# Performance work log

Measured on AMD Instinct MI355X. Metric: run time of the kernel, lower is better.

The kernel has to match this reference:

```python
import jax, jax.numpy as jnp
import numpy as np

B, S, E = 2, 2048, 2048
NQ, NKV, HD = 16, 4, 128
WINDOW = 512
ROPE_BASE = 10000.0


def _rope(x):
    # x: [B, H, S, HD], interleaved even/odd rotation
    half = HD // 2
    freqs = 1.0 / (ROPE_BASE ** (2.0 * jnp.arange(half, dtype=jnp.float32) / HD))
    pos = jnp.arange(x.shape[2], dtype=jnp.float32)
    ang = pos[:, None] * freqs[None, :]            # [S, HD/2]
    cos = jnp.cos(ang)[None, None].astype(x.dtype)  # [1,1,S,HD/2]
    sin = jnp.sin(ang)[None, None].astype(x.dtype)
    xe = x[..., 0::2]
    xo = x[..., 1::2]
    re = xe * cos - xo * sin
    ro = xe * sin + xo * cos
    return jnp.stack([re, ro], axis=-1).reshape(x.shape)


def setup_inputs() -> dict:
    key = jax.random.key(0)
    ks = jax.random.split(key, 9)
    s_in = 1.0 / np.sqrt(E)
    s_out = 1.0 / np.sqrt(NQ * HD)
    return {
        "x": jax.random.normal(ks[0], (B, S, E), jnp.float32),
        "Wq": jax.random.normal(ks[1], (E, NQ * HD), jnp.float32) * s_in,
        "bq": jax.random.normal(ks[2], (NQ * HD,), jnp.float32) * 0.01,
        "Wk": jax.random.normal(ks[3], (E, NKV * HD), jnp.float32) * s_in,
        "bk": jax.random.normal(ks[4], (NKV * HD,), jnp.float32) * 0.01,
        "Wv": jax.random.normal(ks[5], (E, NKV * HD), jnp.float32) * s_in,
        "bv": jax.random.normal(ks[6], (NKV * HD,), jnp.float32) * 0.01,
        "Wo": jax.random.normal(ks[7], (NQ * HD, E), jnp.float32) * s_out,
        "bo": jax.random.normal(ks[8], (E,), jnp.float32) * 0.01,
    }


def reference(x, Wq, bq, Wk, bk, Wv, bv, Wo, bo):
    b, s, _ = x.shape
    q = (x @ Wq + bq).reshape(b, s, NQ, HD).transpose(0, 2, 1, 3)   # [B,NQ,S,HD]
    k = (x @ Wk + bk).reshape(b, s, NKV, HD).transpose(0, 2, 1, 3)  # [B,NKV,S,HD]
    v = (x @ Wv + bv).reshape(b, s, NKV, HD).transpose(0, 2, 1, 3)
    q = _rope(q)
    k = _rope(k)
    rep = NQ // NKV
    k = jnp.repeat(k, rep, axis=1)  # [B,NQ,S,HD], matches torch repeat pattern
    v = jnp.repeat(v, rep, axis=1)
    scores = jnp.einsum("bhqd,bhkd->bhqk", q, k) / np.sqrt(HD)
    i = jnp.arange(s)[:, None]
    j = jnp.arange(s)[None, :]
    allowed = (j <= i) & ((i - j) <= WINDOW)  # sliding-window causal mask
    scores = jnp.where(allowed[None, None], scores, -jnp.inf)
    weights = jax.nn.softmax(scores, axis=-1)
    out = jnp.einsum("bhqk,bhkd->bhqd", weights, v)
    out = out.transpose(0, 2, 1, 3).reshape(b, s, NQ * HD)
    return out @ Wo + bo
```

## Files before the change

### kernel.cpp

```cpp
#include <hip/hip_runtime.h>
#include <hip/hip_bf16.h>
#include <math.h>

#define BB 2
#define SS 2048
#define EE 2048
#define NQ 16
#define NKV 4
#define HD 128
#define WINDOW 512

typedef __hip_bfloat16 bf16;
typedef short short8 __attribute__((ext_vector_type(8)));
typedef float f32x4 __attribute__((ext_vector_type(4)));

__device__ __forceinline__ float toF(bf16 v) { return __bfloat162float(v); }
__device__ __forceinline__ bf16 toB(float v) { return __float2bfloat16(v); }

__device__ __forceinline__ void gld_lds16(const void* g, void* l) {
    __builtin_amdgcn_global_load_lds(
        (const __attribute__((address_space(1))) void*)g,
        (__attribute__((address_space(3))) void*)l, 16, 0, 0);
}

template <int V> __device__ __forceinline__ void waitvm() {
    if constexpr (V == 8)      asm volatile("s_waitcnt vmcnt(8)" ::: "memory");
    else if constexpr (V == 6) asm volatile("s_waitcnt vmcnt(6)" ::: "memory");
    else if constexpr (V == 4) asm volatile("s_waitcnt vmcnt(4)" ::: "memory");
    else if constexpr (V == 3) asm volatile("s_waitcnt vmcnt(3)" ::: "memory");
    else                       asm volatile("s_waitcnt vmcnt(0)" ::: "memory");
}

__global__ __launch_bounds__(256) void convert_bf16(const float* __restrict__ in,
                                                    bf16* __restrict__ out, int n) {
    int i = (blockIdx.x * 256 + threadIdx.x) * 4;
    if (i >= n) return;
    const float4 v = *(const float4*)(in + i);
    bf16 o[4] = {toB(v.x), toB(v.y), toB(v.z), toB(v.w)};
    *(uint2*)(out + i) = *(const uint2*)o;
}

__global__ __launch_bounds__(256) void convert_transpose(const float* __restrict__ in,
                                                         bf16* __restrict__ out,
                                                         int K, int N) {
    __shared__ float tile[32][33];
    const int t = threadIdx.x;
    const int tx = t & 31, ty = t >> 5;
    const int n0 = blockIdx.x * 32, k0 = blockIdx.y * 32;
#pragma unroll
    for (int r = 0; r < 4; r++)
        tile[ty + r * 8][tx] = in[(size_t)(k0 + ty + r * 8) * N + n0 + tx];
    __syncthreads();
#pragma unroll
    for (int r = 0; r < 4; r++)
        out[(size_t)(n0 + ty + r * 8) * K + k0 + tx] = toB(tile[tx][ty + r * 8]);
}

__global__ __launch_bounds__(256) void convert_transpose_qkv(
    const float* __restrict__ Wq, const float* __restrict__ Wk,
    const float* __restrict__ Wv, bf16* __restrict__ out) {
    __shared__ float tile[32][33];
    const int t = threadIdx.x;
    const int tx = t & 31, ty = t >> 5;
    const int n0 = blockIdx.x * 32, k0 = blockIdx.y * 32;
    const float* src; int N, nl0;
    if (n0 < 2048)      { src = Wq; N = 2048; nl0 = n0; }
    else if (n0 < 2560) { src = Wk; N = 512;  nl0 = n0 - 2048; }
    else                { src = Wv; N = 512;  nl0 = n0 - 2560; }
#pragma unroll
    for (int r = 0; r < 4; r++)
        tile[ty + r * 8][tx] = src[(size_t)(k0 + ty + r * 8) * N + nl0 + tx];
    __syncthreads();
#pragma unroll
    for (int r = 0; r < 4; r++)
        out[(size_t)(n0 + ty + r * 8) * 2048 + k0 + tx] = toB(tile[tx][ty + r * 8]);
}

template <int MODE, int BM, int BN>
__global__ __launch_bounds__(512, 2) void mfma_gemm_v4(
    const bf16* __restrict__ A, const bf16* __restrict__ BT,
    const float* __restrict__ b0, const float* __restrict__ b1,
    const float* __restrict__ b2,
    float* __restrict__ Yf,
    bf16* __restrict__ Yq, bf16* __restrict__ Yk, bf16* __restrict__ Yv,
    int M, int N, int K) {
    constexpr int NI = BM / 32;
    constexpr int NJ = BN / 64;
    constexpr int LA = BM / 128;
    constexpr int LB = BN / 128;
    constexpr int SL = LA + LB;

    __shared__ __align__(16) bf16 As[4][BM * 32];
    __shared__ __align__(16) bf16 Bs[4][BN * 32];

    const int t = threadIdx.x;
    const int lane = t & 63;
    const int w = t >> 6;
    const int wm = w >> 2;
    const int wn = w & 3;
    const int m0 = blockIdx.y * BM, n0 = blockIdx.x * BN;
    const int lr = lane & 15;
    const int lq = lane >> 4;
    const int NT = K >> 5;

    auto stage = [&](int s) {
        bf16* Ad = &As[s & 3][0];
#pragma unroll
        for (int l = 0; l < LA; l++) {
            const int c = w * LA + l;
            const int row = c * 16 + (lane >> 2);
            const int g = (lane & 3) ^ ((row >> 1) & 3);
            gld_lds16(A + (size_t)(m0 + row) * K + s * 32 + g * 8, Ad + c * 512);
        }
        bf16* Bd = &Bs[s & 3][0];
#pragma unroll
        for (int l = 0; l < LB; l++) {
            const int c = w * LB + l;
            const int row = c * 16 + (lane >> 2);
            const int g = (lane & 3) ^ ((row >> 1) & 3);
            gld_lds16(BT + (size_t)(n0 + row) * K + s * 32 + g * 8, Bd + c * 512);
        }
    };

    auto loadfr = [&](int s, short8 (&fA)[NI], short8 (&fB)[NJ]) {
        const bf16* Asl = &As[s & 3][0];
        const bf16* Bsl = &Bs[s & 3][0];
#pragma unroll
        for (int i = 0; i < NI; i++) {
            const int row = wm * (NI * 16) + i * 16 + lr;
            const int sl = lq ^ ((row >> 1) & 3);
            fA[i] = *(const short8*)(Asl + row * 32 + sl * 8);
        }
#pragma unroll
        for (int j = 0; j < NJ; j++) {
            const int row = wn * (NJ * 16) + j * 16 + lr;
            const int sl = lq ^ ((row >> 1) & 3);
            fB[j] = *(const short8*)(Bsl + row * 32 + sl * 8);
        }
    };

    f32x4 acc[NI][NJ];
#pragma unroll
    for (int i = 0; i < NI; i++)
#pragma unroll
        for (int j = 0; j < NJ; j++) acc[i][j] = (f32x4)0.f;

    auto region = [&](int r, short8 (&fAc)[NI], short8 (&fBc)[NJ],
                             short8 (&fAn)[NI], short8 (&fBn)[NJ]) {
        if (r + 3 < NT) stage(r + 3);
        if (r + 1 < NT) loadfr(r + 1, fAn, fBn);
        __builtin_amdgcn_sched_barrier(0);
        __builtin_amdgcn_s_setprio(1);
#pragma unroll
        for (int i = 0; i < NI; i++)
#pragma unroll
            for (int j = 0; j < NJ; j++)
                acc[i][j] = __builtin_amdgcn_mfma_f32_16x16x32_bf16(fAc[i], fBc[j],
                                                                    acc[i][j], 0, 0, 0);
        __builtin_amdgcn_s_setprio(0);
        asm volatile("s_waitcnt lgkmcnt(0)" ::: "memory");
        if (r + 3 < NT) waitvm<SL>(); else waitvm<0>();
        __builtin_amdgcn_sched_barrier(0);
        __builtin_amdgcn_s_barrier();
    };

    stage(0); stage(1); stage(2);
    waitvm<SL>();
    __builtin_amdgcn_s_barrier();
    short8 fA0[NI], fB0[NJ], fA1[NI], fB1[NJ];
    loadfr(0, fA0, fB0);
    asm volatile("s_waitcnt lgkmcnt(0)" ::: "memory");
    __builtin_amdgcn_sched_barrier(0);

    for (int r = 0; r < NT; r += 2) {
        region(r,     fA0, fB0, fA1, fB1);
        region(r + 1, fA1, fB1, fA0, fB0);
    }

    if (MODE == 0) {
#pragma unroll
        for (int j = 0; j < NJ; j++) {
            const int col = n0 + wn * (NJ * 16) + j * 16 + lr;
            const float bj = b0[col];
#pragma unroll
            for (int i = 0; i < NI; i++) {
                const int row = m0 + wm * (NI * 16) + i * 16 + lq * 4;
#pragma unroll
                for (int r = 0; r < 4; r++)
                    Yf[(size_t)(row + r) * N + col] = acc[i][j][r] + bj;
            }
        }
    } else {
#pragma unroll
        for (int j = 0; j < NJ; j++) {
            const int gcol = n0 + wn * (NJ * 16) + j * 16 + lr;
            if (gcol < 2560) {
                bf16* outp; const float* bias; int ldc, col;
                if (gcol < 2048) { outp = Yq; bias = b0; ldc = 2048; col = gcol; }
                else             { outp = Yk; bias = b1; ldc = 512;  col = gcol - 2048; }
                const float bj = bias[col];
                const int d2 = (col & 127) >> 1;
                const bool odd = col & 1;
                const float freq = __expf(-0.14384103622589045f * (float)d2);
#pragma unroll
                for (int i = 0; i < NI; i++) {
                    const int row = m0 + wm * (NI * 16) + i * 16 + lq * 4;
#pragma unroll
                    for (int r = 0; r < 4; r++) {
                        const float v = acc[i][j][r] + bj;
                        const float p = __shfl_xor(v, 1, 64);
                        const float ang = (float)((row + r) & (SS - 1)) * freq;
                        float sn, cs;
                        __sincosf(ang, &sn, &cs);
                        const float o = odd ? (p * sn + v * cs) : (v * cs - p * sn);
                        outp[(size_t)(row + r) * ldc + col] = toB(o);
                    }
                }
            } else {
                const int col = gcol - 2560;
                const float bj = b2[col];
                const int hkv = col >> 7, d = col & 127;
#pragma unroll
                for (int i = 0; i < NI; i++) {
                    const int row = m0 + wm * (NI * 16) + i * 16 + lq * 4;
                    const int bb = row >> 11, sr = row & (SS - 1);
                    union { bf16 b[4]; uint2 u; } o4;
#pragma unroll
                    for (int r = 0; r < 4; r++) o4.b[r] = toB(acc[i][j][r] + bj);
                    *(uint2*)(Yv + (((size_t)bb * NKV + hkv) * HD + d) * SS + sr) = o4.u;
                }
            }
        }
    }
}

__global__ __launch_bounds__(256) void attn_mfma(const bf16* __restrict__ Q,
                                                 const bf16* __restrict__ K,
                                                 const bf16* __restrict__ VT,
                                                 bf16* __restrict__ Oout) {
    __shared__ bf16 Ks[64 * 128];
    __shared__ bf16 Vs[128 * 64];
    __shared__ bf16 Ps[4 * 16 * 72];

    const int t = threadIdx.x;
    const int lane = t & 63;
    const int w = t >> 6;
    const int q0 = blockIdx.x * 64;
    const int h = blockIdx.y;
    const int b = blockIdx.z;
    const int hkv = h >> 2;
    const int lr = lane & 15;
    const int lq = lane >> 4;
    const float scale = 0.08838834764831845f;

    short8 aq[4];
    {
        const int q = q0 + w * 16 + lr;
        const bf16* qp = Q + (((size_t)b * SS + q) * NQ + h) * HD + lq * 8;
#pragma unroll
        for (int ks = 0; ks < 4; ks++) aq[ks] = *(const short8*)(qp + ks * 32);
    }

    const int krow = w * 16 + (lane >> 4);
    const int vrow = w * 32 + (lane >> 3);
    const bf16* Kbase = K + ((size_t)b * SS * NKV + hkv) * HD;
    const bf16* Vbase = VT + (((size_t)b * NKV + hkv) * HD) * SS;

    f32x4 Oa[8];
#pragma unroll
    for (int nb = 0; nb < 8; nb++) Oa[nb] = (f32x4)0.f;
    float mprev[4] = {-3.0e38f, -3.0e38f, -3.0e38f, -3.0e38f};
    float lsum[4] = {0.f, 0.f, 0.f, 0.f};

    bf16* Pw = Ps + w * 16 * 72;
    const int jstart = (q0 >= WINDOW) ? (q0 - WINDOW) : 0;

    for (int c0 = jstart; c0 <= q0; c0 += 64) {
        __syncthreads();
#pragma unroll
        for (int s = 0; s < 4; s++) {
            const int r_ = krow + s * 4;
            const int g_ = (lane & 15) ^ (r_ & 7);
            gld_lds16(Kbase + (size_t)(c0 + r_) * (NKV * HD) + g_ * 8,
                      Ks + (w * 16 + s * 4) * 128);
        }
#pragma unroll
        for (int s = 0; s < 4; s++) {
            const int d_ = vrow + s * 8;
            const int g_ = (lane & 7) ^ (d_ & 7);
            gld_lds16(Vbase + (size_t)d_ * SS + c0 + g_ * 8,
                      Vs + (w * 32 + s * 8) * 64);
        }
        __syncthreads();

        f32x4 sa[4];
#pragma unroll
        for (int nb = 0; nb < 4; nb++) sa[nb] = (f32x4)0.f;
#pragma unroll
        for (int ks = 0; ks < 4; ks++) {
#pragma unroll
            for (int nb = 0; nb < 4; nb++) {
                const int slot = (ks * 4 + lq) ^ (lr & 7);
                short8 bk = *(const short8*)(Ks + (nb * 16 + lr) * 128 + slot * 8);
                sa[nb] = __builtin_amdgcn_mfma_f32_16x16x32_bf16(aq[ks], bk, sa[nb], 0, 0, 0);
            }
        }

        const int rowb = q0 + w * 16 + lq * 4;
        const bool noMask = (c0 + 63 <= q0 + w * 16) &&
                            (q0 + w * 16 + 15 - c0 <= WINDOW);
        float pr[4][4], alpha[4];
#pragma unroll
        for (int r = 0; r < 4; r++) {
            const int row = rowb + r;
            float sv[4];
            float mx = -3.0e38f;
            if (noMask) {
#pragma unroll
                for (int nb = 0; nb < 4; nb++) {
                    const float s = sa[nb][r] * scale;
                    sv[nb] = s;
                    mx = fmaxf(mx, s);
                }
            } else {
#pragma unroll
                for (int nb = 0; nb < 4; nb++) {
                    const int col = c0 + nb * 16 + lr;
                    const bool valid = (col <= row) && (row - col <= WINDOW);
                    const float s = valid ? sa[nb][r] * scale : -3.0e38f;
                    sv[nb] = s;
                    mx = fmaxf(mx, s);
                }
            }
#pragma unroll
            for (int off = 1; off < 16; off <<= 1) mx = fmaxf(mx, __shfl_xor(mx, off, 64));
            const float mn = fmaxf(fmaxf(mprev[r], mx), -1.0e30f);
            alpha[r] = __expf(mprev[r] - mn);
            mprev[r] = mn;
            float rs = 0.f;
#pragma unroll
            for (int nb = 0; nb < 4; nb++) {
                const float p = __expf(sv[nb] - mn);
                pr[r][nb] = p;
                rs += p;
            }
#pragma unroll
            for (int off = 1; off < 16; off <<= 1) rs += __shfl_xor(rs, off, 64);
            lsum[r] = lsum[r] * alpha[r] + rs;
        }

#pragma unroll
        for (int r = 0; r < 4; r++)
#pragma unroll
            for (int nb = 0; nb < 4; nb++)
                Pw[(lq * 4 + r) * 72 + nb * 16 + lr] = toB(pr[r][nb]);

#pragma unroll
        for (int nb = 0; nb < 8; nb++)
#pragma unroll
            for (int r = 0; r < 4; r++) Oa[nb][r] *= alpha[r];
#pragma unroll
        for (int ks = 0; ks < 2; ks++) {
            short8 pa = *(const short8*)(Pw + lr * 72 + ks * 32 + lq * 8);
#pragma unroll
            for (int nb = 0; nb < 8; nb++) {
                const int slot = (ks * 4 + lq) ^ (lr & 7);
                short8 bv = *(const short8*)(Vs + (nb * 16 + lr) * 64 + slot * 8);
                Oa[nb] = __builtin_amdgcn_mfma_f32_16x16x32_bf16(pa, bv, Oa[nb], 0, 0, 0);
            }
        }
    }

    float linv[4];
#pragma unroll
    for (int r = 0; r < 4; r++) linv[r] = 1.f / lsum[r];
    const int rowb = q0 + w * 16 + lq * 4;
#pragma unroll
    for (int nb = 0; nb < 8; nb++)
#pragma unroll
        for (int r = 0; r < 4; r++)
            Oout[(((size_t)b * SS + rowb + r) * NQ + h) * HD + nb * 16 + lr] =
                toB(Oa[nb][r] * linv[r]);
}

extern "C" void kernel_launch(void* const* d_in, const int* in_sizes, int n_in,
                              void* d_out, int out_size, void* d_ws, size_t ws_size,
                              hipStream_t stream) {
    const float* x  = (const float*)d_in[0];
    const float* Wq = (const float*)d_in[1];
    const float* bq = (const float*)d_in[2];
    const float* Wk = (const float*)d_in[3];
    const float* bk = (const float*)d_in[4];
    const float* Wv = (const float*)d_in[5];
    const float* bv = (const float*)d_in[6];
    const float* Wo = (const float*)d_in[7];
    const float* bo = (const float*)d_in[8];
    float* out = (float*)d_out;

    const int M   = BB * SS;
    const int DQ  = NQ * HD;
    const int DKV = NKV * HD;
    const int NPK = DQ + 2 * DKV;

    bf16* xb     = (bf16*)d_ws;
    bf16* WqkvT  = xb + (size_t)M * EE;
    bf16* WoT    = WqkvT + (size_t)NPK * EE;
    bf16* Qb     = WoT + (size_t)EE * DQ;
    bf16* Kb     = Qb + (size_t)M * DQ;
    bf16* Vb     = Kb + (size_t)M * DKV;

    convert_bf16<<<(M * EE / 4 + 255) / 256, 256, 0, stream>>>(x, xb, M * EE);
    convert_transpose_qkv<<<dim3(NPK / 32, EE / 32), 256, 0, stream>>>(Wq, Wk, Wv, WqkvT);
    convert_transpose<<<dim3(DQ / 32, DQ / 32), 256, 0, stream>>>(Wo, WoT, DQ, EE);

    mfma_gemm_v4<1, 128, 384><<<dim3(NPK / 384, M / 128), 512, 0, stream>>>(
        xb, WqkvT, bq, bk, bv, nullptr, Qb, Kb, Vb, M, NPK, EE);

    attn_mfma<<<dim3(SS / 64, NQ, BB), 256, 0, stream>>>(Qb, Kb, Vb, Qb);

    mfma_gemm_v4<0, 128, 256><<<dim3(EE / 256, M / 128), 512, 0, stream>>>(
        Qb, WoT, bo, nullptr, nullptr, out, nullptr, nullptr, nullptr, M, EE, DQ);
}
```

Measured before the change: 332.8 us.

## Rework GEMM pipeline to BK=64 triple buffer with XCD-aware tile mapping

The GEMM kernel now loads K tiles 64 wide instead of 32, into a 3-stage LDS ring instead of a 4-stage one, with an 8-slot XOR swizzle. Each K tile is split into two sub-k fragment reads that are interleaved with MFMA clusters, so there is one barrier per 64 of K rather than per 32. Block indices are remapped so that consecutive M tiles land on the same XCD, which should improve L2 reuse of the B operand. The QKV GEMM also moves from 384-wide to 192-wide N tiles, which doubles its grid, and the wait counts and tile-size math change to match.

```diff
diff --git a/kernel.cpp b/kernel.cpp
--- a/kernel.cpp
+++ b/kernel.cpp
@@ -26,9 +26,13 @@
 template <int V> __device__ __forceinline__ void waitvm() {
     if constexpr (V == 8)      asm volatile("s_waitcnt vmcnt(8)" ::: "memory");
     else if constexpr (V == 6) asm volatile("s_waitcnt vmcnt(6)" ::: "memory");
+    else if constexpr (V == 5) asm volatile("s_waitcnt vmcnt(5)" ::: "memory");
     else if constexpr (V == 4) asm volatile("s_waitcnt vmcnt(4)" ::: "memory");
     else if constexpr (V == 3) asm volatile("s_waitcnt vmcnt(3)" ::: "memory");
     else                       asm volatile("s_waitcnt vmcnt(0)" ::: "memory");
+}
+__device__ __forceinline__ void waitlgkm0() {
+    asm volatile("s_waitcnt lgkmcnt(0)" ::: "memory");
 }
 
 __global__ __launch_bounds__(256) void convert_bf16(const float* __restrict__ in,
@@ -77,65 +81,77 @@
 }
 
 template <int MODE, int BM, int BN>
-__global__ __launch_bounds__(512, 2) void mfma_gemm_v4(
+__global__ __launch_bounds__(512, 2) void mfma_gemm_v6(
     const bf16* __restrict__ A, const bf16* __restrict__ BT,
     const float* __restrict__ b0, const float* __restrict__ b1,
     const float* __restrict__ b2,
     float* __restrict__ Yf,
     bf16* __restrict__ Yq, bf16* __restrict__ Yk, bf16* __restrict__ Yv,
     int M, int N, int K) {
-    constexpr int NI = BM / 32;
-    constexpr int NJ = BN / 64;
-    constexpr int LA = BM / 128;
-    constexpr int LB = BN / 128;
+    constexpr int NI = BM / 2 / 16;
+    constexpr int NJ = BN / 4 / 16;
+    constexpr int LA = BM / 64;
+    constexpr int LB = BN / 64;
     constexpr int SL = LA + LB;
 
-    __shared__ __align__(16) bf16 As[4][BM * 32];
-    __shared__ __align__(16) bf16 Bs[4][BN * 32];
-
-    const int t = threadIdx.x;
-    const int lane = t & 63;
-    const int w = t >> 6;
+    __shared__ __align__(16) bf16 As[3][BM * 64];
+    __shared__ __align__(16) bf16 Bs[3][BN * 64];
+
+    const int tid = threadIdx.x;
+    const int lane = tid & 63;
+    const int w = tid >> 6;
     const int wm = w >> 2;
     const int wn = w & 3;
-    const int m0 = blockIdx.y * BM, n0 = blockIdx.x * BN;
+
+    const int gx = gridDim.x, gy = gridDim.y;
+    const int lin = blockIdx.y * gx + blockIdx.x;
+    const int xcd = lin & 7;
+    const int idx = lin >> 3;
+    const int rpx = gy >> 3;
+    const int tn = idx / rpx;
+    const int tm = xcd * rpx + (idx % rpx);
+    const int m0 = tm * BM, n0 = tn * BN;
+
     const int lr = lane & 15;
     const int lq = lane >> 4;
-    const int NT = K >> 5;
+    const int NT = K >> 6;
+
+    const int srow = tid >> 3;
+    const int sslot = tid & 7;
 
     auto stage = [&](int s) {
-        bf16* Ad = &As[s & 3][0];
+        bf16* Ad = &As[s % 3][0];
 #pragma unroll
         for (int l = 0; l < LA; l++) {
-            const int c = w * LA + l;
-            const int row = c * 16 + (lane >> 2);
-            const int g = (lane & 3) ^ ((row >> 1) & 3);
-            gld_lds16(A + (size_t)(m0 + row) * K + s * 32 + g * 8, Ad + c * 512);
-        }
-        bf16* Bd = &Bs[s & 3][0];
+            const int row = l * 64 + srow;
+            const int g = sslot ^ (row & 7);
+            gld_lds16(A + (size_t)(m0 + row) * K + s * 64 + g * 8,
+                      Ad + l * 4096 + w * 512);
+        }
+        bf16* Bd = &Bs[s % 3][0];
 #pragma unroll
         for (int l = 0; l < LB; l++) {
-            const int c = w * LB + l;
-            const int row = c * 16 + (lane >> 2);
-            const int g = (lane & 3) ^ ((row >> 1) & 3);
-            gld_lds16(BT + (size_t)(n0 + row) * K + s * 32 + g * 8, Bd + c * 512);
+            const int row = l * 64 + srow;
+            const int g = sslot ^ (row & 7);
+            gld_lds16(BT + (size_t)(n0 + row) * K + s * 64 + g * 8,
+                      Bd + l * 4096 + w * 512);
         }
     };
 
-    auto loadfr = [&](int s, short8 (&fA)[NI], short8 (&fB)[NJ]) {
-        const bf16* Asl = &As[s & 3][0];
-        const bf16* Bsl = &Bs[s & 3][0];
+    auto readf = [&](int s, int kk, short8 (&fA)[NI], short8 (&fB)[NJ]) {
+        const bf16* Asl = &As[s % 3][0];
+        const bf16* Bsl = &Bs[s % 3][0];
 #pragma unroll
         for (int i = 0; i < NI; i++) {
             const int row = wm * (NI * 16) + i * 16 + lr;
-            const int sl = lq ^ ((row >> 1) & 3);
-            fA[i] = *(const short8*)(Asl + row * 32 + sl * 8);
+            const int sl = ((kk << 2) | lq) ^ (row & 7);
+            fA[i] = *(const short8*)(Asl + row * 64 + sl * 8);
         }
 #pragma unroll
         for (int j = 0; j < NJ; j++) {
             const int row = wn * (NJ * 16) + j * 16 + lr;
-            const int sl = lq ^ ((row >> 1) & 3);
-            fB[j] = *(const short8*)(Bsl + row * 32 + sl * 8);
+            const int sl = ((kk << 2) | lq) ^ (row & 7);
+            fB[j] = *(const short8*)(Bsl + row * 64 + sl * 8);
         }
     };
 
@@ -145,36 +161,34 @@
 #pragma unroll
         for (int j = 0; j < NJ; j++) acc[i][j] = (f32x4)0.f;
 
-    auto region = [&](int r, short8 (&fAc)[NI], short8 (&fBc)[NJ],
-                             short8 (&fAn)[NI], short8 (&fBn)[NJ]) {
-        if (r + 3 < NT) stage(r + 3);
-        if (r + 1 < NT) loadfr(r + 1, fAn, fBn);
-        __builtin_amdgcn_sched_barrier(0);
+    auto cluster = [&](short8 (&fA)[NI], short8 (&fB)[NJ]) {
         __builtin_amdgcn_s_setprio(1);
 #pragma unroll
         for (int i = 0; i < NI; i++)
 #pragma unroll
             for (int j = 0; j < NJ; j++)
-                acc[i][j] = __builtin_amdgcn_mfma_f32_16x16x32_bf16(fAc[i], fBc[j],
+                acc[i][j] = __builtin_amdgcn_mfma_f32_16x16x32_bf16(fA[i], fB[j],
                                                                     acc[i][j], 0, 0, 0);
         __builtin_amdgcn_s_setprio(0);
-        asm volatile("s_waitcnt lgkmcnt(0)" ::: "memory");
-        if (r + 3 < NT) waitvm<SL>(); else waitvm<0>();
-        __builtin_amdgcn_sched_barrier(0);
-        __builtin_amdgcn_s_barrier();
     };
 
-    stage(0); stage(1); stage(2);
+    stage(0); stage(1);
     waitvm<SL>();
     __builtin_amdgcn_s_barrier();
+    __builtin_amdgcn_sched_barrier(0);
     short8 fA0[NI], fB0[NJ], fA1[NI], fB1[NJ];
-    loadfr(0, fA0, fB0);
-    asm volatile("s_waitcnt lgkmcnt(0)" ::: "memory");
-    __builtin_amdgcn_sched_barrier(0);
-
-    for (int r = 0; r < NT; r += 2) {
-        region(r,     fA0, fB0, fA1, fB1);
-        region(r + 1, fA1, fB1, fA0, fB0);
+    readf(0, 0, fA0, fB0);
+
+    for (int t = 0; t < NT; ++t) {
+        if (t + 2 < NT) stage(t + 2);
+        readf(t, 1, fA1, fB1);
+        cluster(fA0, fB0);
+        waitlgkm0();
+        if (t + 2 < NT) waitvm<SL>(); else waitvm<0>();
+        __builtin_amdgcn_s_barrier();
+        __builtin_amdgcn_sched_barrier(0);
+        if (t + 1 < NT) readf(t + 1, 0, fA0, fB0);
+        cluster(fA1, fB1);
     }
 
     if (MODE == 0) {
@@ -413,11 +427,11 @@
     convert_transpose_qkv<<<dim3(NPK / 32, EE / 32), 256, 0, stream>>>(Wq, Wk, Wv, WqkvT);
     convert_transpose<<<dim3(DQ / 32, DQ / 32), 256, 0, stream>>>(Wo, WoT, DQ, EE);
 
-    mfma_gemm_v4<1, 128, 384><<<dim3(NPK / 384, M / 128), 512, 0, stream>>>(
+    mfma_gemm_v6<1, 128, 192><<<dim3(NPK / 192, M / 128), 512, 0, stream>>>(
         xb, WqkvT, bq, bk, bv, nullptr, Qb, Kb, Vb, M, NPK, EE);
 
     attn_mfma<<<dim3(SS / 64, NQ, BB), 256, 0, stream>>>(Qb, Kb, Vb, Qb);
 
-    mfma_gemm_v4<0, 128, 256><<<dim3(EE / 256, M / 128), 512, 0, stream>>>(
+    mfma_gemm_v6<0, 128, 256><<<dim3(EE / 256, M / 128), 512, 0, stream>>>(
         Qb, WoT, bo, nullptr, nullptr, out, nullptr, nullptr, nullptr, M, EE, DQ);
 }
```

After: 312.6 us. 1.06x faster.
